# Kernel tuning notes

Hardware: AMD Instinct MI355X
Metric: run time of the kernel (lower is better)

## Reference

```python
import jax, jax.numpy as jnp
import numpy as np

MAX_DISPLACEMENT = 4  # matches init_kwargs
EPS = 1e-12  # torch F.normalize clamp


def _l2_normalize(x):
    # L2 normalize over channel dim (axis=1), matching torch.nn.functional.normalize
    n = jnp.sqrt(jnp.sum(x * x, axis=1, keepdims=True))
    return x / jnp.maximum(n, EPS)


def setup_inputs() -> dict:
    key = jax.random.key(0)
    k1, k2 = jax.random.split(key)
    B, C, H, W = 16, 256, 64, 64
    fA = jax.random.normal(k1, (B, C, H, W), dtype=jnp.float32)
    fB = jax.random.normal(k2, (B, C, H, W), dtype=jnp.float32)
    return {"fA": fA, "fB": fB}


def reference(fA, fB):
    d = MAX_DISPLACEMENT
    B, C, H, W = fA.shape
    fAn = _l2_normalize(fA)
    fBn = _l2_normalize(fB)
    # zero-pad fB by d (matches F.unfold padding=d), then take shifted windows.
    fBp = jnp.pad(fBn, ((0, 0), (0, 0), (d, d), (d, d)))
    outs = []
    # Fixed structural loop over (2d+1)^2 = 81 displacements (row-major ky, kx,
    # matching F.unfold's kernel-position ordering). No huge patch tensor is
    # materialized; each term is a channel dot-product of fA with shifted fB.
    for dy in range(2 * d + 1):
        for dx in range(2 * d + 1):
            shifted = jax.lax.dynamic_slice(
                fBp, (0, 0, dy, dx), (B, C, H, W))
            outs.append(jnp.sum(fAn * shifted, axis=1))  # (B, H, W)
    return jnp.stack(outs, axis=1)  # (B, (2d+1)^2, H, W)
```

## Files before the change

### kernel.cpp

```cpp
#include <hip/hip_runtime.h>
#include <hip/hip_bf16.h>
#include <math.h>

typedef short short8 __attribute__((ext_vector_type(8)));
typedef float f32x16 __attribute__((ext_vector_type(16)));

#define BB 16
#define CC 256
#define HH 64
#define WW 64
#define HWX 4096
#define DD 4
#define KD 9
#define KK 81
#define NSLOT 10

__device__ __forceinline__ short bf16c(float x) {
    __hip_bfloat16 h = __float2bfloat16(x);
    return *reinterpret_cast<short*>(&h);
}

__device__ __forceinline__ void b_issue16(const float* __restrict__ row,
                                          int c0, int l, float* v) {
    #pragma unroll
    for (int j = 0; j < 16; ++j)
        v[j] = row[(size_t)(c0 + j) * HWX + l];
}

__device__ __forceinline__ float b_commit16(const float* v, unsigned short* bufp,
                                            int c0, int l) {
    float ss = 0.f;
    #pragma unroll
    for (int j = 0; j < 16; ++j) ss += v[j] * v[j];
    #pragma unroll
    for (int ch = 0; ch < 2; ++ch) {
        short8 st;
        #pragma unroll
        for (int j = 0; j < 8; ++j) st[j] = bf16c(v[ch * 8 + j]);
        const int c = c0 + ch * 8;
        const int byte = (l * 512 + c * 2) ^ ((l & 31) << 4);
        *(short8*)((char*)bufp + byte) = st;
    }
    return ss;
}

__global__ __launch_bounds__(512) void corr_mfma(
    const float* __restrict__ fA, const float* __restrict__ fB,
    float* __restrict__ out)
{
    __shared__ __attribute__((aligned(16))) unsigned short buf[2][WW * CC];
    __shared__ float red[2][2][KD][WW + 1];
    __shared__ float part[2][8 * WW];

    const int bid = blockIdx.x;
    const int swzb = (bid & 7) * 64 + (bid >> 3);
    const int b = swzb >> 5, jr = swzb & 31;
    const int h0 = 2 * jr;

    const int tid = threadIdx.x;
    const int wv = tid >> 6, l = tid & 63;
    const int g = wv >> 2;
    const int q = wv & 3;
    const int hg = h0 + g;
    const int ti = q >> 1, tj = q & 1;
    const int ml = l & 31, kg = l >> 5;
    const int m = ti * 32 + ml;
    const int n = tj * 32 + ml;

    const float* Abase = fA + (size_t)b * CC * HWX + hg * WW;
    {
        float ss = 0.f;
        #pragma unroll
        for (int r = 0; r < 8; ++r) {
            float v[8];
            #pragma unroll
            for (int j = 0; j < 8; ++j) v[j] = Abase[(size_t)(q * 64 + r * 8 + j) * HWX + l];
            #pragma unroll
            for (int j = 0; j < 8; ++j) ss += v[j] * v[j];
        }
        part[1][wv * 64 + l] = ss;
    }
    __syncthreads();
    float iaA;
    {
        float s = part[1][(g * 4 + 0) * 64 + l] + part[1][(g * 4 + 1) * 64 + l]
                + part[1][(g * 4 + 2) * 64 + l] + part[1][(g * 4 + 3) * 64 + l];
        iaA = 1.f / fmaxf(sqrtf(s), 1e-12f);
    }
    for (int i = tid; i < 2 * 2 * KD * (WW + 1); i += 512) ((float*)red)[i] = 0.f;
    #pragma unroll
    for (int r = 0; r < 8; ++r) {
        const int c = q * 64 + r * 8;
        float v[8]; short8 st;
        #pragma unroll
        for (int j = 0; j < 8; ++j) v[j] = Abase[(size_t)(c + j) * HWX + l];
        #pragma unroll
        for (int j = 0; j < 8; ++j) st[j] = bf16c(v[j] * iaA);
        const int byte = (l * 512 + c * 2) ^ ((l & 31) << 4);
        *(short8*)((char*)buf[g] + byte) = st;
    }
    __syncthreads();
    short8 afr[16];
    #pragma unroll
    for (int s = 0; s < 16; ++s) {
        const int byte = (m * 512 + s * 32 + kg * 16) ^ ((m & 31) << 4);
        afr[s] = *(const short8*)((const char*)buf[g] + byte);
    }
    __syncthreads();

    const float* fBb = fB + (size_t)b * CC * HWX;
    {
        const int hb0 = h0 - DD;
        if ((unsigned)hb0 < HH) {
            const float* row = fBb + (size_t)hb0 * WW;
            float v[16];
            b_issue16(row, wv * 32, l, v);
            float ss = b_commit16(v, buf[0], wv * 32, l);
            b_issue16(row, wv * 32 + 16, l, v);
            ss += b_commit16(v, buf[0], wv * 32 + 16, l);
            part[0][wv * 64 + l] = ss;
        }
    }
    __syncthreads();

    for (int r = 0; r < NSLOT; ++r) {
        const int cur = r & 1;
        const int hb = h0 - DD + r;
        const bool vcur = (unsigned)hb < HH;
        const bool vnext = (r + 1 < NSLOT) && ((unsigned)(hb + 1) < HH);
        const float* nrow = fBb + (size_t)(hb + 1) * WW;
        const int dy = r - g;
        const bool dyv = (dy >= 0 && dy < KD);

        float v[16];
        if (vnext) b_issue16(nrow, wv * 32, l, v);

        if (r >= 1) {
            const int dyp = (r - 1) - g;
            if (dyp >= 0 && dyp < KD) {
                const int tid2 = q * 64 + l;
                float* ob = out + (((size_t)b * KK + dyp * KD) * HH + hg) * WW;
                for (int i = tid2; i < KD * WW; i += 256)
                    ob[(size_t)(i >> 6) * HWX + (i & 63)] = red[g][cur ^ 1][i >> 6][i & 63];
            }
        }

        f32x16 acc;
        const bool comp = dyv && vcur;
        if (comp) {
            #pragma unroll
            for (int i = 0; i < 16; ++i) acc[i] = 0.f;
            #pragma unroll
            for (int s = 0; s < 8; ++s) {
                const int byte = (n * 512 + s * 32 + kg * 16) ^ ((n & 31) << 4);
                short8 bfr = *(const short8*)((const char*)buf[cur] + byte);
                acc = __builtin_amdgcn_mfma_f32_32x32x16_bf16(afr[s], bfr, acc, 0, 0, 0);
            }
        }

        float ssn = 0.f;
        if (vnext) {
            ssn = b_commit16(v, buf[cur ^ 1], wv * 32, l);
            b_issue16(nrow, wv * 32 + 16, l, v);
        }

        if (comp) {
            #pragma unroll
            for (int s = 8; s < 16; ++s) {
                const int byte = (n * 512 + s * 32 + kg * 16) ^ ((n & 31) << 4);
                short8 bfr = *(const short8*)((const char*)buf[cur] + byte);
                acc = __builtin_amdgcn_mfma_f32_32x32x16_bf16(afr[s], bfr, acc, 0, 0, 0);
            }
            float sB = 0.f;
            #pragma unroll
            for (int qq = 0; qq < 8; ++qq) sB += part[cur][qq * 64 + n];
            const float ibn = 1.f / fmaxf(sqrtf(sB), 1e-12f);
            #pragma unroll
            for (int rr = 0; rr < 16; ++rr) {
                const int w = ti * 32 + (rr & 3) + 8 * (rr >> 2) + 4 * kg;
                const int dx = n - w + 4;
                if (dx >= 0 && dx < KD) red[g][cur][dx][w] = acc[rr] * ibn;
            }
        } else if (dyv) {
            #pragma unroll
            for (int rr = 0; rr < 16; ++rr) {
                const int w = ti * 32 + (rr & 3) + 8 * (rr >> 2) + 4 * kg;
                const int dx = n - w + 4;
                if (dx >= 0 && dx < KD) red[g][cur][dx][w] = 0.f;
            }
        }

        if (vnext) {
            ssn += b_commit16(v, buf[cur ^ 1], wv * 32 + 16, l);
            part[cur ^ 1][wv * 64 + l] = ssn;
        }
        __syncthreads();
    }

    {
        const int dyp = (NSLOT - 1) - g;
        if (dyp >= 0 && dyp < KD) {
            const int tid2 = q * 64 + l;
            float* ob = out + (((size_t)b * KK + dyp * KD) * HH + hg) * WW;
            for (int i = tid2; i < KD * WW; i += 256)
                ob[(size_t)(i >> 6) * HWX + (i & 63)] = red[g][(NSLOT - 1) & 1][i >> 6][i & 63];
        }
    }
}

extern "C" void kernel_launch(void* const* d_in, const int* in_sizes, int n_in,
                              void* d_out, int out_size, void* d_ws, size_t ws_size,
                              hipStream_t stream) {
    const float* fA = (const float*)d_in[0];
    const float* fB = (const float*)d_in[1];
    float* outp = (float*)d_out;
    corr_mfma<<<dim3(BB * HH / 2), 512, 0, stream>>>(fA, fB, outp);
}
```

Measured before the change: 64.93 us.

## Process four output rows per block to reuse staged fB rows more

Each block now handles 4 output rows with 1024 threads instead of 2 rows with 512. That cuts the number of fB rows loaded and normalized per output row: 12 slots serve 4 rows, where 10 slots served 2 before. Because LDS only has room for two A rows at a time, A-fragment staging is split into two rounds. Each thread now loads 8 channels of B instead of 16. The MFMA sections are also bracketed with s_setprio. The trade-off is fewer, larger blocks with a tighter register budget per thread (the 16 A fragments plus the accumulator under a 1024-thread bound), which could cause spills or lower latency hiding.

```diff
diff --git a/kernel.cpp b/kernel.cpp
--- a/kernel.cpp
+++ b/kernel.cpp
@@ -13,54 +13,52 @@
 #define DD 4
 #define KD 9
 #define KK 81
-#define NSLOT 10
+#define GR 4
+#define NSLOT 12
 
 __device__ __forceinline__ short bf16c(float x) {
     __hip_bfloat16 h = __float2bfloat16(x);
     return *reinterpret_cast<short*>(&h);
 }
 
-__device__ __forceinline__ void b_issue16(const float* __restrict__ row,
-                                          int c0, int l, float* v) {
-    #pragma unroll
-    for (int j = 0; j < 16; ++j)
+__device__ __forceinline__ void b_issue8(const float* __restrict__ row,
+                                         int c0, int l, float* v) {
+    #pragma unroll
+    for (int j = 0; j < 8; ++j)
         v[j] = row[(size_t)(c0 + j) * HWX + l];
 }
 
-__device__ __forceinline__ float b_commit16(const float* v, unsigned short* bufp,
-                                            int c0, int l) {
+__device__ __forceinline__ float b_commit8(const float* v, unsigned short* bufp,
+                                           int c0, int l) {
     float ss = 0.f;
     #pragma unroll
-    for (int j = 0; j < 16; ++j) ss += v[j] * v[j];
-    #pragma unroll
-    for (int ch = 0; ch < 2; ++ch) {
-        short8 st;
-        #pragma unroll
-        for (int j = 0; j < 8; ++j) st[j] = bf16c(v[ch * 8 + j]);
-        const int c = c0 + ch * 8;
-        const int byte = (l * 512 + c * 2) ^ ((l & 31) << 4);
-        *(short8*)((char*)bufp + byte) = st;
-    }
+    for (int j = 0; j < 8; ++j) ss += v[j] * v[j];
+    short8 st;
+    #pragma unroll
+    for (int j = 0; j < 8; ++j) st[j] = bf16c(v[j]);
+    const int byte = (l * 512 + c0 * 2) ^ ((l & 31) << 4);
+    *(short8*)((char*)bufp + byte) = st;
     return ss;
 }
 
-__global__ __launch_bounds__(512) void corr_mfma(
+__global__ __launch_bounds__(1024) void corr_mfma(
     const float* __restrict__ fA, const float* __restrict__ fB,
     float* __restrict__ out)
 {
     __shared__ __attribute__((aligned(16))) unsigned short buf[2][WW * CC];
-    __shared__ float red[2][2][KD][WW + 1];
-    __shared__ float part[2][8 * WW];
+    __shared__ float red[GR][2][KD][WW + 1];
+    __shared__ float part[2][16 * WW];
 
     const int bid = blockIdx.x;
-    const int swzb = (bid & 7) * 64 + (bid >> 3);
-    const int b = swzb >> 5, jr = swzb & 31;
-    const int h0 = 2 * jr;
+    const int swzb = (bid & 7) * 32 + (bid >> 3);
+    const int b = swzb >> 4, jr = swzb & 15;
+    const int h0 = 4 * jr;
 
     const int tid = threadIdx.x;
-    const int wv = tid >> 6, l = tid & 63;
-    const int g = wv >> 2;
-    const int q = wv & 3;
+    const int l = tid & 63;
+    const int wvu = __builtin_amdgcn_readfirstlane(tid >> 6);
+    const int g = wvu >> 2;
+    const int q = wvu & 3;
     const int hg = h0 + g;
     const int ti = q >> 1, tj = q & 1;
     const int ml = l & 31, kg = l >> 5;
@@ -78,47 +76,55 @@
             #pragma unroll
             for (int j = 0; j < 8; ++j) ss += v[j] * v[j];
         }
-        part[1][wv * 64 + l] = ss;
+        part[1][wvu * 64 + l] = ss;
     }
     __syncthreads();
     float iaA;
     {
-        float s = part[1][(g * 4 + 0) * 64 + l] + part[1][(g * 4 + 1) * 64 + l]
-                + part[1][(g * 4 + 2) * 64 + l] + part[1][(g * 4 + 3) * 64 + l];
-        iaA = 1.f / fmaxf(sqrtf(s), 1e-12f);
-    }
-    for (int i = tid; i < 2 * 2 * KD * (WW + 1); i += 512) ((float*)red)[i] = 0.f;
-    #pragma unroll
-    for (int r = 0; r < 8; ++r) {
-        const int c = q * 64 + r * 8;
-        float v[8]; short8 st;
-        #pragma unroll
-        for (int j = 0; j < 8; ++j) v[j] = Abase[(size_t)(c + j) * HWX + l];
-        #pragma unroll
-        for (int j = 0; j < 8; ++j) st[j] = bf16c(v[j] * iaA);
-        const int byte = (l * 512 + c * 2) ^ ((l & 31) << 4);
-        *(short8*)((char*)buf[g] + byte) = st;
-    }
-    __syncthreads();
+        const int gb = g * 4;
+        iaA = 1.f / fmaxf(sqrtf(part[1][(gb + 0) * 64 + l] + part[1][(gb + 1) * 64 + l]
+                              + part[1][(gb + 2) * 64 + l] + part[1][(gb + 3) * 64 + l]), 1e-12f);
+    }
+    for (int i = tid; i < GR * 2 * KD * (WW + 1); i += 1024) ((float*)red)[i] = 0.f;
+
     short8 afr[16];
     #pragma unroll
-    for (int s = 0; s < 16; ++s) {
-        const int byte = (m * 512 + s * 32 + kg * 16) ^ ((m & 31) << 4);
-        afr[s] = *(const short8*)((const char*)buf[g] + byte);
-    }
-    __syncthreads();
+    for (int round = 0; round < 2; ++round) {
+        if ((g >> 1) == round) {
+            #pragma unroll
+            for (int r = 0; r < 8; ++r) {
+                const int c = q * 64 + r * 8;
+                float v[8]; short8 st;
+                #pragma unroll
+                for (int j = 0; j < 8; ++j) v[j] = Abase[(size_t)(c + j) * HWX + l];
+                #pragma unroll
+                for (int j = 0; j < 8; ++j) st[j] = bf16c(v[j] * iaA);
+                const int byte = (l * 512 + c * 2) ^ ((l & 31) << 4);
+                *(short8*)((char*)buf[g & 1] + byte) = st;
+            }
+        }
+        __syncthreads();
+        if ((g >> 1) == round) {
+            #pragma unroll
+            for (int s = 0; s < 16; ++s) {
+                const int byte = (m * 512 + s * 32 + kg * 16) ^ ((m & 31) << 4);
+                afr[s] = *(const short8*)((const char*)buf[g & 1] + byte);
+            }
+        }
+        __syncthreads();
+    }
 
     const float* fBb = fB + (size_t)b * CC * HWX;
     {
         const int hb0 = h0 - DD;
         if ((unsigned)hb0 < HH) {
             const float* row = fBb + (size_t)hb0 * WW;
-            float v[16];
-            b_issue16(row, wv * 32, l, v);
-            float ss = b_commit16(v, buf[0], wv * 32, l);
-            b_issue16(row, wv * 32 + 16, l, v);
-            ss += b_commit16(v, buf[0], wv * 32 + 16, l);
-            part[0][wv * 64 + l] = ss;
+            float v[8];
+            b_issue8(row, wvu * 16, l, v);
+            float ss = b_commit8(v, buf[0], wvu * 16, l);
+            b_issue8(row, wvu * 16 + 8, l, v);
+            ss += b_commit8(v, buf[0], wvu * 16 + 8, l);
+            part[0][wvu * 64 + l] = ss;
         }
     }
     __syncthreads();
@@ -131,9 +137,10 @@
         const float* nrow = fBb + (size_t)(hb + 1) * WW;
         const int dy = r - g;
         const bool dyv = (dy >= 0 && dy < KD);
-
-        float v[16];
-        if (vnext) b_issue16(nrow, wv * 32, l, v);
+        const bool comp = dyv && vcur;
+
+        float v[8];
+        if (vnext) b_issue8(nrow, wvu * 16, l, v);
 
         if (r >= 1) {
             const int dyp = (r - 1) - g;
@@ -146,34 +153,37 @@
         }
 
         f32x16 acc;
-        const bool comp = dyv && vcur;
         if (comp) {
             #pragma unroll
             for (int i = 0; i < 16; ++i) acc[i] = 0.f;
+            __builtin_amdgcn_s_setprio(1);
             #pragma unroll
             for (int s = 0; s < 8; ++s) {
                 const int byte = (n * 512 + s * 32 + kg * 16) ^ ((n & 31) << 4);
                 short8 bfr = *(const short8*)((const char*)buf[cur] + byte);
                 acc = __builtin_amdgcn_mfma_f32_32x32x16_bf16(afr[s], bfr, acc, 0, 0, 0);
             }
+            __builtin_amdgcn_s_setprio(0);
         }
 
         float ssn = 0.f;
         if (vnext) {
-            ssn = b_commit16(v, buf[cur ^ 1], wv * 32, l);
-            b_issue16(nrow, wv * 32 + 16, l, v);
+            ssn = b_commit8(v, buf[cur ^ 1], wvu * 16, l);
+            b_issue8(nrow, wvu * 16 + 8, l, v);
         }
 
         if (comp) {
+            __builtin_amdgcn_s_setprio(1);
             #pragma unroll
             for (int s = 8; s < 16; ++s) {
                 const int byte = (n * 512 + s * 32 + kg * 16) ^ ((n & 31) << 4);
                 short8 bfr = *(const short8*)((const char*)buf[cur] + byte);
                 acc = __builtin_amdgcn_mfma_f32_32x32x16_bf16(afr[s], bfr, acc, 0, 0, 0);
             }
+            __builtin_amdgcn_s_setprio(0);
             float sB = 0.f;
             #pragma unroll
-            for (int qq = 0; qq < 8; ++qq) sB += part[cur][qq * 64 + n];
+            for (int w16 = 0; w16 < 16; ++w16) sB += part[cur][w16 * 64 + n];
             const float ibn = 1.f / fmaxf(sqrtf(sB), 1e-12f);
             #pragma unroll
             for (int rr = 0; rr < 16; ++rr) {
@@ -191,8 +201,8 @@
         }
 
         if (vnext) {
-            ssn += b_commit16(v, buf[cur ^ 1], wv * 32 + 16, l);
-            part[cur ^ 1][wv * 64 + l] = ssn;
+            ssn += b_commit8(v, buf[cur ^ 1], wvu * 16 + 8, l);
+            part[cur ^ 1][wvu * 64 + l] = ssn;
         }
         __syncthreads();
     }
@@ -214,5 +224,5 @@
     const float* fA = (const float*)d_in[0];
     const float* fB = (const float*)d_in[1];
     float* outp = (float*)d_out;
-    corr_mfma<<<dim3(BB * HH / 2), 512, 0, stream>>>(fA, fB, outp);
-}
+    corr_mfma<<<dim3(BB * HH / GR), 1024, 0, stream>>>(fA, fB, outp);
+}
```

Result: slower. 140.2 us (+115.9%).
